# Optimization experiments

Hardware: AMD Instinct MI355X
Metric: run time of the kernel (lower is better)

Reference implementation:

```python
import jax, jax.numpy as jnp
import numpy as np

jax.config.update("jax_enable_x64", True)  # original computes distances in float64

B, NL, NP, C, H, G, A, E = 16, 64, 512, 128, 256, 10, 14, 2048
BN_EPS = 1e-5


def _static_indices():
    # ragged graph sizes (batch_num_nodes) -> static scatter / valid-pair indices
    counts_l = np.array([32 if i % 2 == 0 else 64 for i in range(B)])
    counts_p = np.array([256 if i % 2 == 0 else 512 for i in range(B)])
    idx_l = np.concatenate([b * NL + np.arange(c) for b, c in enumerate(counts_l)])
    idx_p = np.concatenate([b * NP + np.arange(c) for b, c in enumerate(counts_p)])
    mask_l = np.zeros(B * NL, bool); mask_l[idx_l] = True
    mask_p = np.zeros(B * NP, bool); mask_p[idx_p] = True
    mask = mask_l.reshape(B, NL, 1) & mask_p.reshape(B, 1, NP)  # C_mask
    pair_flat = np.nonzero(mask.reshape(-1))[0]                 # row-major == torch C[C_mask] order
    pb = pair_flat // (NL * NP)
    rem = pair_flat % (NL * NP)
    pair_l = pb * NL + rem // NP
    pair_p = pb * NP + rem % NP
    return idx_l, idx_p, pair_flat, pair_l, pair_p, pb, len(idx_l), len(idx_p)


def setup_inputs() -> dict:
    idx_l, idx_p, pair_flat, pair_l, pair_p, pair_b, TL, TP = _static_indices()
    ks = jax.random.split(jax.random.key(0), 14)
    f32 = jnp.float32
    s = 0.02
    return {
        "h_l": jax.random.normal(ks[0], (TL, C), f32),
        "h_p": jax.random.normal(ks[1], (TP, C), f32),
        "lig_pos": jax.random.normal(ks[2], (TL, 3), f32) * 5.0,
        "prot_pos": jax.random.normal(ks[3], (TP, A, 3), f32) * 5.0,
        "edge_src": jax.random.randint(ks[4], (E,), 0, TL),
        "edge_dst": jax.random.randint(ks[5], (E,), 0, TL),
        "idx_l": jnp.asarray(idx_l), "idx_p": jnp.asarray(idx_p),
        "pair_flat": jnp.asarray(pair_flat), "pair_l": jnp.asarray(pair_l),
        "pair_p": jnp.asarray(pair_p), "pair_b": jnp.asarray(pair_b),
        "W1": jax.random.normal(ks[6], (2 * C, H), f32) * s, "b1": jnp.zeros(H, f32),
        "gamma": jnp.ones(H, f32), "beta": jnp.zeros(H, f32),
        "rmean": jnp.zeros(H, f32), "rvar": jnp.ones(H, f32),
        "Wpi": jax.random.normal(ks[7], (H, G * A), f32) * s, "bpi": jnp.zeros(G * A, f32),
        "Wsig": jax.random.normal(ks[8], (H, G * A), f32) * s, "bsig": jnp.zeros(G * A, f32),
        "Wmu": jax.random.normal(ks[9], (H, G * A), f32) * s, "bmu": jnp.zeros(G * A, f32),
        "Wat": jax.random.normal(ks[10], (C, 17), f32) * s, "bat": jnp.zeros(17, f32),
        "Wbt": jax.random.normal(ks[11], (2 * C, 5), f32) * s, "bbt": jnp.zeros(5, f32),
    }


def reference(h_l, h_p, lig_pos, prot_pos, edge_src, edge_dst, idx_l, idx_p,
              pair_flat, pair_l, pair_p, pair_b, W1, b1, gamma, beta, rmean, rvar,
              Wpi, bpi, Wsig, bsig, Wmu, bmu, Wat, bat, Wbt, bbt):
    # scatter ragged node feats into padded dense batches (to_dense_batch_dgl)
    dense_l = jnp.zeros((B * NL, C), h_l.dtype).at[idx_l].set(h_l)
    dense_p = jnp.zeros((B * NP, C), h_p.dtype).at[idx_p].set(h_p)
    # gather only valid (ligand, protein) pairs instead of the dense [B,NL,NP,2C] tensor
    Cpair = jnp.concatenate([dense_l[pair_l], dense_p[pair_p]], axis=-1)  # [M, 2C]
    x = Cpair @ W1 + b1
    x = gamma * (x - rmean) / jnp.sqrt(rvar + BN_EPS) + beta  # BatchNorm1d (eval)
    x = jax.nn.elu(x)                                          # dropout off (eval)
    pi = jax.nn.softmax(x @ Wpi + bpi, axis=-1).reshape(-1, G, A)
    sigma = (jax.nn.elu(x @ Wsig + bsig) + 1.1).reshape(-1, G, A)
    mu = (jax.nn.elu(x @ Wmu + bmu) + 1.0).reshape(-1, G, A)
    atom_types = h_l @ Wat + bat                               # [TL, 17]
    bond_types = jnp.concatenate([h_l[edge_src], h_l[edge_dst]], -1) @ Wbt + bbt  # [E, 5]
    # euclidean distance matrix in float64, as in the original
    X = jnp.zeros((B * NL, 3), jnp.float64).at[idx_l].set(lig_pos.astype(jnp.float64)).reshape(B, NL, 3)
    Y = jnp.zeros((B * NP, A, 3), jnp.float64).at[idx_p].set(prot_pos.astype(jnp.float64)).reshape(B, NP * A, 3)
    d2 = (-2.0 * jnp.einsum('bld,bpd->blp', X, Y)
          + jnp.sum(Y * Y, -1)[:, None, :] + jnp.sum(X * X, -1)[:, :, None])
    dist = jnp.nan_to_num(jnp.sqrt(d2), nan=10000.0).reshape(B * NL * NP, A)[pair_flat]
    dist = jax.lax.stop_gradient(dist[:, None, :])             # [M, 1, A], detached
    return (pi, sigma, mu, dist, atom_types, bond_types, pair_b)
```

## Files before the change

### kernel.cpp

```cpp
#include <hip/hip_runtime.h>


typedef __attribute__((ext_vector_type(4))) float f32x4;
typedef __attribute__((ext_vector_type(4))) unsigned int u32x4;
typedef __attribute__((ext_vector_type(8))) short bf16x8;

#define M_TOT 327680
#define WSCALE 16.0f
#define WDESCALE 0.0625f

__device__ __forceinline__ unsigned short f2bf(float f) {
    union { float f; unsigned int u; } v; v.f = f;
    unsigned int r = (v.u + 0x7FFFu + ((v.u >> 16) & 1u)) >> 16;
    return (unsigned short)r;
}

__device__ __forceinline__ float eluf(float y) {
    return fmaxf(y, 0.f) + __expf(fminf(y, 0.f)) - 1.f;
}

__device__ __forceinline__ float bfhalf_lo(unsigned int u) {
    return __uint_as_float(u << 16);
}
__device__ __forceinline__ float bfhalf_hi(unsigned int u) {
    return __uint_as_float(u & 0xFFFF0000u);
}

__device__ __forceinline__ void pair_decode(int m0, int& b, int& cl, int& cp0) {
    unsigned int P = (unsigned int)m0 / 40960u;
    unsigned int r = (unsigned int)m0 % 40960u;
    if (r < 8192u) {
        b = 2 * (int)P; cl = 96 * (int)P + (int)(r >> 8); cp0 = 768 * (int)P + (int)(r & 255u);
    } else {
        unsigned int rr = r - 8192u;
        b = 2 * (int)P + 1; cl = 96 * (int)P + 32 + (int)(rr >> 9);
        cp0 = 768 * (int)P + 256 + (int)(rr & 511u);
    }
}

__global__ void setup_kernel(const float* __restrict__ W1, const float* __restrict__ b1,
                             const float* __restrict__ gamma, const float* __restrict__ beta,
                             const float* __restrict__ rmean, const float* __restrict__ rvar,
                             const float* __restrict__ Wpi, const float* __restrict__ bpi,
                             const float* __restrict__ Wsig, const float* __restrict__ bsig,
                             const float* __restrict__ Wmu, const float* __restrict__ bmu,
                             const float* __restrict__ h_l,
                             const int* __restrict__ esrc, const int* __restrict__ edst,
                             const float* __restrict__ Wat, const float* __restrict__ bat,
                             const float* __restrict__ Wbt, const float* __restrict__ bbt,
                             const float* __restrict__ lig_pos, const float* __restrict__ prot_pos,
                             unsigned short* __restrict__ W1T, unsigned char* __restrict__ W2q,
                             float* __restrict__ b2s, float* __restrict__ a1v, float* __restrict__ csv,
                             float* __restrict__ out_at, float* __restrict__ out_bt,
                             float* __restrict__ out_dist, float* __restrict__ out_pb) {
    if (blockIdx.x >= 432) {
        const int m0 = (blockIdx.x - 432) * 256;
        int b, cl, cp0;
        pair_decode(m0, b, cl, cp0);
        const int rw = threadIdx.x;
        float lx = lig_pos[cl * 3 + 0];
        float ly = lig_pos[cl * 3 + 1];
        float lz = lig_pos[cl * 3 + 2];
        const float* pp = prot_pos + (size_t)(cp0 + rw) * 42;
        float* dr = out_dist + (size_t)(m0 + rw) * 14;
        #pragma unroll
        for (int a = 0; a < 14; ++a) {
            float dx = lx - pp[a * 3 + 0];
            float dy = ly - pp[a * 3 + 1];
            float dz = lz - pp[a * 3 + 2];
            dr[a] = sqrtf(dx * dx + dy * dy + dz * dz);
        }
        out_pb[m0 + rw] = (float)b;
        return;
    }

    int idx = blockIdx.x * 256 + threadIdx.x;
    {
        int j    = idx & 7;
        int h    = (idx >> 3) & 1;
        int lane = (idx >> 4) & 63;
        int sp   = (idx >> 10) & 3;
        int t    = idx >> 12;
        int f    = t % 9;
        int head = t / 9;
        int k    = (sp * 2 + h) * 32 + (lane >> 4) * 8 + j;
        int col  = f * 16 + (lane & 15);
        float v = 0.f;
        if (col < 140) {
            const float* Wh = (head == 0) ? Wpi : (head == 1) ? Wsig : Wmu;
            v = Wh[k * 140 + col] * WSCALE;
        }
        W2q[idx] = (unsigned char)(__builtin_amdgcn_cvt_pk_fp8_f32(v, 0.f, 0, false) & 0xFF);
    }
    if (idx < 256 * 256) {
        int n = idx & 255, k = idx >> 8;
        W1T[n * 256 + k] = f2bf(W1[k * 256 + n]);
    }
    if (idx < 432) {
        int head = idx / 144, col = idx % 144;
        float v = 0.f;
        if (col < 140) v = (head == 0) ? bpi[col] : (head == 1) ? bsig[col] : bmu[col];
        b2s[idx] = v * WSCALE;
    }
    if (idx < 256) {
        float s = gamma[idx] * rsqrtf(rvar[idx] + 1e-5f);
        a1v[idx] = s;
        csv[idx] = s * (b1[idx] - rmean[idx]) + beta[idx];
    }
    if (idx < 768 * 17) {
        int row = idx / 17, c = idx % 17;
        const float* hr = h_l + (size_t)row * 128;
        float s = bat[c];
        #pragma unroll 4
        for (int k = 0; k < 128; ++k) s += hr[k] * Wat[k * 17 + c];
        out_at[idx] = s;
    } else if (idx < 768 * 17 + 2048 * 5) {
        int t2 = idx - 768 * 17;
        int e = t2 / 5, c = t2 % 5;
        const float* hs = h_l + (size_t)esrc[e] * 128;
        const float* hd = h_l + (size_t)edst[e] * 128;
        float s = bbt[c];
        #pragma unroll 4
        for (int k = 0; k < 128; ++k)
            s += hs[k] * Wbt[k * 5 + c] + hd[k] * Wbt[(k + 128) * 5 + c];
        out_bt[t2] = s;
    }
}

__global__ __launch_bounds__(256, 2) void node_gemm(
        const float* __restrict__ h_l, const float* __restrict__ h_p,
        const unsigned short* __restrict__ W1T,
        const float* __restrict__ a1v, const float* __restrict__ csv,
        unsigned short* __restrict__ Lq, unsigned short* __restrict__ Pq) {
    const int tid = threadIdx.x, lane = tid & 63, w = tid >> 6;
    const int cGrp = lane & 15, g = lane >> 4;
    const int nh   = blockIdx.x & 1;
    const int row0 = (blockIdx.x >> 1) * 64;
    const bool isLig = row0 < 768;
    const float* src = isLig ? (h_l + (size_t)row0 * 128) : (h_p + (size_t)(row0 - 768) * 128);
    unsigned short* dst = isLig ? (Lq + (size_t)row0 * 256) : (Pq + (size_t)(row0 - 768) * 256);
    const int koff = isLig ? 0 : 128;

    f32x4 acc[8];
    #pragma unroll
    for (int fn = 0; fn < 8; ++fn) acc[fn] = (f32x4){0.f, 0.f, 0.f, 0.f};

    #pragma unroll
    for (int fk = 0; fk < 4; ++fk) {
        const float* ap = src + (size_t)(w * 16 + cGrp) * 128 + fk * 32 + g * 8;
        f32x4 qa = *(const f32x4*)ap;
        f32x4 qb = *(const f32x4*)(ap + 4);
        bf16x8 af;
        af[0] = (short)f2bf(qa[0]); af[1] = (short)f2bf(qa[1]);
        af[2] = (short)f2bf(qa[2]); af[3] = (short)f2bf(qa[3]);
        af[4] = (short)f2bf(qb[0]); af[5] = (short)f2bf(qb[1]);
        af[6] = (short)f2bf(qb[2]); af[7] = (short)f2bf(qb[3]);
        #pragma unroll
        for (int fn = 0; fn < 8; ++fn) {
            int n = nh * 128 + fn * 16 + cGrp;
            bf16x8 bf = *(const bf16x8*)(W1T + (size_t)n * 256 + koff + fk * 32 + g * 8);
            acc[fn] = __builtin_amdgcn_mfma_f32_16x16x32_bf16(af, bf, acc[fn], 0, 0, 0);
        }
    }
    #pragma unroll
    for (int fn = 0; fn < 8; ++fn) {
        int h = nh * 128 + fn * 16 + cGrp;
        float s = a1v[h];
        float c0 = isLig ? csv[h] : 0.f;
        #pragma unroll
        for (int rg = 0; rg < 4; ++rg)
            dst[(size_t)(w * 16 + g * 4 + rg) * 256 + h] = f2bf(s * acc[fn][rg] + c0);
    }
}

__global__ __launch_bounds__(256, 4) void pair_kernel(
        const unsigned short* __restrict__ Lq, const unsigned short* __restrict__ Pq,
        const unsigned char* __restrict__ W2q, const float* __restrict__ b2s,
        float* __restrict__ out_pi, float* __restrict__ out_sig, float* __restrict__ out_mu) {

    __shared__ __align__(16) unsigned char Bs[36864];

    const int tid = threadIdx.x, lane = tid & 63, w = tid >> 6;
    const int c = lane & 15, g = lane >> 4;
    const int m0 = blockIdx.x * 64;

    int b, cl, cp0;
    pair_decode(m0, b, cl, cp0);

    u32x4 stg[9];
    #pragma unroll
    for (int i = 0; i < 9; ++i)
        stg[i] = *(const u32x4*)(W2q + (size_t)(tid + 256 * i) * 16);

    const int row = w * 16 + c;
    const unsigned short* pqp = Pq + (size_t)(cp0 + row) * 256;
    const unsigned short* lqp = Lq + (size_t)cl * 256;
    long Xa[8];
    #pragma unroll
    for (int s = 0; s < 8; ++s) {
        u32x4 pv = *(const u32x4*)(pqp + s * 32 + g * 8);
        u32x4 lv = *(const u32x4*)(lqp + s * 32 + g * 8);
        float y0 = eluf(bfhalf_lo(pv[0]) + bfhalf_lo(lv[0]));
        float y1 = eluf(bfhalf_hi(pv[0]) + bfhalf_hi(lv[0]));
        float y2 = eluf(bfhalf_lo(pv[1]) + bfhalf_lo(lv[1]));
        float y3 = eluf(bfhalf_hi(pv[1]) + bfhalf_hi(lv[1]));
        float y4 = eluf(bfhalf_lo(pv[2]) + bfhalf_lo(lv[2]));
        float y5 = eluf(bfhalf_hi(pv[2]) + bfhalf_hi(lv[2]));
        float y6 = eluf(bfhalf_lo(pv[3]) + bfhalf_lo(lv[3]));
        float y7 = eluf(bfhalf_hi(pv[3]) + bfhalf_hi(lv[3]));
        unsigned int lo = (unsigned int)__builtin_amdgcn_cvt_pk_fp8_f32(y0, y1, 0, false);
        lo = (unsigned int)__builtin_amdgcn_cvt_pk_fp8_f32(y2, y3, (int)lo, true);
        unsigned int hi = (unsigned int)__builtin_amdgcn_cvt_pk_fp8_f32(y4, y5, 0, false);
        hi = (unsigned int)__builtin_amdgcn_cvt_pk_fp8_f32(y6, y7, (int)hi, true);
        Xa[s] = (long)(((unsigned long long)hi << 32) | (unsigned long long)lo);
    }

    const bool v8 = (c < 12);

    #pragma unroll
    for (int head = 0; head < 3; ++head) {
        #pragma unroll
        for (int i = 0; i < 9; ++i)
            *(u32x4*)(Bs + (size_t)(tid + 256 * i) * 16) = stg[i];
        __syncthreads();

        float bb[9];
        #pragma unroll
        for (int f = 0; f < 9; ++f) bb[f] = b2s[head * 144 + f * 16 + c];

        f32x4 acc[9];
        #pragma unroll
        for (int f = 0; f < 9; ++f) acc[f] = (f32x4){bb[f], bb[f], bb[f], bb[f]};

        #pragma unroll
        for (int sp = 0; sp < 4; ++sp) {
            long xa0 = Xa[2 * sp], xa1 = Xa[2 * sp + 1];
            #pragma unroll
            for (int f = 0; f < 9; ++f) {
                u32x4 bq = *(const u32x4*)(Bs + f * 4096 + sp * 1024 + lane * 16);
                long b0 = (long)(((unsigned long long)bq[1] << 32) | (unsigned long long)bq[0]);
                long b1 = (long)(((unsigned long long)bq[3] << 32) | (unsigned long long)bq[2]);
                acc[f] = __builtin_amdgcn_mfma_f32_16x16x32_fp8_fp8(xa0, b0, acc[f], 0, 0, 0);
                acc[f] = __builtin_amdgcn_mfma_f32_16x16x32_fp8_fp8(xa1, b1, acc[f], 0, 0, 0);
            }
        }

        if (head < 2) {
            const unsigned char* wsrc = W2q + (size_t)(head + 1) * 36864;
            #pragma unroll
            for (int i = 0; i < 9; ++i)
                stg[i] = *(const u32x4*)(wsrc + (size_t)(tid + 256 * i) * 16);
        }

        #pragma unroll
        for (int f = 0; f < 9; ++f)
            #pragma unroll
            for (int q = 0; q < 4; ++q) acc[f][q] *= WDESCALE;

        if (head == 0) {
            #pragma unroll
            for (int q = 0; q < 4; ++q) {
                float e0 = __expf(acc[0][q]), e1 = __expf(acc[1][q]);
                float e2 = __expf(acc[2][q]), e3 = __expf(acc[3][q]);
                float e4 = __expf(acc[4][q]), e5 = __expf(acc[5][q]);
                float e6 = __expf(acc[6][q]), e7 = __expf(acc[7][q]);
                float e8 = v8 ? __expf(acc[8][q]) : 0.f;
                float sm = ((e0 + e1) + (e2 + e3)) + ((e4 + e5) + (e6 + e7)) + e8;
                sm += __shfl_xor(sm, 1, 64);
                sm += __shfl_xor(sm, 2, 64);
                sm += __shfl_xor(sm, 4, 64);
                sm += __shfl_xor(sm, 8, 64);
                float inv = 1.f / sm;
                acc[0][q] = e0 * inv; acc[1][q] = e1 * inv;
                acc[2][q] = e2 * inv; acc[3][q] = e3 * inv;
                acc[4][q] = e4 * inv; acc[5][q] = e5 * inv;
                acc[6][q] = e6 * inv; acc[7][q] = e7 * inv;
                acc[8][q] = e8 * inv;
            }
        } else {
            const float addc = (head == 1) ? 1.1f : 1.0f;
            #pragma unroll
            for (int f = 0; f < 9; ++f)
                #pragma unroll
                for (int q = 0; q < 4; ++q) acc[f][q] = eluf(acc[f][q]) + addc;
        }

        __syncthreads();
        float* ot = (float*)Bs;
        {
            const int rbase = (w * 16 + g * 4) * 140 + c;
            #pragma unroll
            for (int f = 0; f < 9; ++f) {
                if (f < 8 || v8) {
                    #pragma unroll
                    for (int q = 0; q < 4; ++q)
                        ot[rbase + q * 140 + f * 16] = acc[f][q];
                }
            }
        }
        __syncthreads();

        float* dsth = (head == 0) ? out_pi : (head == 1) ? out_sig : out_mu;
        float* dst = dsth + (size_t)m0 * 140;
        #pragma unroll
        for (int i = 0; i < 9; ++i) {
            int idx = tid + 256 * i;
            if (idx < 2240)
                *(f32x4*)(dst + idx * 4) = *(const f32x4*)(ot + idx * 4);
        }

        if (head < 2) __syncthreads();
    }
}

extern "C" void kernel_launch(void* const* d_in, const int* in_sizes, int n_in,
                              void* d_out, int out_size, void* d_ws, size_t ws_size,
                              hipStream_t stream) {
    const float* h_l      = (const float*)d_in[0];
    const float* h_p      = (const float*)d_in[1];
    const float* lig_pos  = (const float*)d_in[2];
    const float* prot_pos = (const float*)d_in[3];
    const int*   esrc     = (const int*)d_in[4];
    const int*   edst     = (const int*)d_in[5];
    const float* W1    = (const float*)d_in[12];
    const float* b1    = (const float*)d_in[13];
    const float* gamma = (const float*)d_in[14];
    const float* beta  = (const float*)d_in[15];
    const float* rmean = (const float*)d_in[16];
    const float* rvar  = (const float*)d_in[17];
    const float* Wpi   = (const float*)d_in[18];
    const float* bpi   = (const float*)d_in[19];
    const float* Wsig  = (const float*)d_in[20];
    const float* bsig  = (const float*)d_in[21];
    const float* Wmu   = (const float*)d_in[22];
    const float* bmu   = (const float*)d_in[23];
    const float* Wat   = (const float*)d_in[24];
    const float* bat   = (const float*)d_in[25];
    const float* Wbt   = (const float*)d_in[26];
    const float* bbt   = (const float*)d_in[27];

    char* ws = (char*)d_ws;
    unsigned short* W1T = (unsigned short*)(ws + 0);
    unsigned char*  W2q = (unsigned char*)(ws + 131072);
    float*          b2s = (float*)(ws + 241664);
    float*          a1v = (float*)(ws + 243392);
    float*          csv = (float*)(ws + 244416);
    unsigned short* Lq  = (unsigned short*)(ws + 245440);
    unsigned short* Pq  = (unsigned short*)(ws + 638656);

    float* out = (float*)d_out;
    const size_t M = M_TOT;
    float* out_pi   = out;
    float* out_sig  = out + M * 140;
    float* out_mu   = out + 2 * M * 140;
    float* out_dist = out + 3 * M * 140;
    float* out_at   = out + 3 * M * 140 + M * 14;
    float* out_bt   = out_at + 768 * 17;
    float* out_pb   = out_bt + 2048 * 5;

    hipLaunchKernelGGL(setup_kernel, dim3(432 + M_TOT / 256), dim3(256), 0, stream,
                       W1, b1, gamma, beta, rmean, rvar,
                       Wpi, bpi, Wsig, bsig, Wmu, bmu,
                       h_l, esrc, edst, Wat, bat, Wbt, bbt,
                       lig_pos, prot_pos,
                       W1T, W2q, b2s, a1v, csv, out_at, out_bt, out_dist, out_pb);

    hipLaunchKernelGGL(node_gemm, dim3(2 * (768 + 6144) / 64), dim3(256), 0, stream,
                       h_l, h_p, W1T, a1v, csv, Lq, Pq);

    hipLaunchKernelGGL(pair_kernel, dim3(M_TOT / 64), dim3(256), 0, stream,
                       Lq, Pq, W2q, b2s, out_pi, out_sig, out_mu);
}
```

Measured before the change: 176.4 us.

## Fold node GEMM into setup kernel with per-block LDS W1 transpose

Merges the node_gemm kernel into setup_kernel as extra blocks. Each node block converts and transposes its 128x128 slice of W1 to bf16 in shared memory and computes the batch-norm scale and shift inline, instead of reading a global W1T and the a1v/csv buffers produced by the setup pass. This removes one kernel launch and the dependency between the two kernels, letting the node GEMM overlap with the distance and prep work. The cost is redundant W1 conversion in every node block and 34KB of LDS allocated for all blocks of setup_kernel, which may lower occupancy for the distance blocks.

```diff
diff --git a/kernel.cpp b/kernel.cpp
--- a/kernel.cpp
+++ b/kernel.cpp
@@ -8,6 +8,10 @@
 #define M_TOT 327680
 #define WSCALE 16.0f
 #define WDESCALE 0.0625f
+
+#define NODE_BLOCKS 216
+#define PREP_BLOCKS 432
+#define DIST_BLOCKS 1280
 
 __device__ __forceinline__ unsigned short f2bf(float f) {
     union { float f; unsigned int u; } v; v.f = f;
@@ -44,20 +48,80 @@
                              const float* __restrict__ Wpi, const float* __restrict__ bpi,
                              const float* __restrict__ Wsig, const float* __restrict__ bsig,
                              const float* __restrict__ Wmu, const float* __restrict__ bmu,
-                             const float* __restrict__ h_l,
+                             const float* __restrict__ h_l, const float* __restrict__ h_p,
                              const int* __restrict__ esrc, const int* __restrict__ edst,
                              const float* __restrict__ Wat, const float* __restrict__ bat,
                              const float* __restrict__ Wbt, const float* __restrict__ bbt,
                              const float* __restrict__ lig_pos, const float* __restrict__ prot_pos,
-                             unsigned short* __restrict__ W1T, unsigned char* __restrict__ W2q,
-                             float* __restrict__ b2s, float* __restrict__ a1v, float* __restrict__ csv,
+                             unsigned char* __restrict__ W2q, float* __restrict__ b2s,
+                             unsigned short* __restrict__ Lq, unsigned short* __restrict__ Pq,
                              float* __restrict__ out_at, float* __restrict__ out_bt,
                              float* __restrict__ out_dist, float* __restrict__ out_pb) {
-    if (blockIdx.x >= 432) {
-        const int m0 = (blockIdx.x - 432) * 256;
+
+    __shared__ __align__(16) unsigned short Wl[128 * 136];
+
+    const int bid = blockIdx.x;
+    const int tid = threadIdx.x;
+
+    if (bid < NODE_BLOCKS) {
+        const int nh   = bid & 1;
+        const int row0 = (bid >> 1) * 64;
+        const bool isLig = row0 < 768;
+        const float* src = isLig ? (h_l + (size_t)row0 * 128) : (h_p + (size_t)(row0 - 768) * 128);
+        unsigned short* dst = isLig ? (Lq + (size_t)row0 * 256) : (Pq + (size_t)(row0 - 768) * 256);
+        const int koff = isLig ? 0 : 128;
+
+        {
+            const int nn = tid & 127;
+            const int kb = tid >> 7;
+            #pragma unroll 8
+            for (int i = 0; i < 64; ++i) {
+                int kk = i * 2 + kb;
+                Wl[nn * 136 + kk] = f2bf(W1[(size_t)(koff + kk) * 256 + nh * 128 + nn]);
+            }
+        }
+        __syncthreads();
+
+        const int lane = tid & 63, w = tid >> 6;
+        const int cGrp = lane & 15, g = lane >> 4;
+
+        f32x4 acc[8];
+        #pragma unroll
+        for (int fn = 0; fn < 8; ++fn) acc[fn] = (f32x4){0.f, 0.f, 0.f, 0.f};
+
+        #pragma unroll
+        for (int fk = 0; fk < 4; ++fk) {
+            const float* ap = src + (size_t)(w * 16 + cGrp) * 128 + fk * 32 + g * 8;
+            f32x4 qa = *(const f32x4*)ap;
+            f32x4 qb = *(const f32x4*)(ap + 4);
+            bf16x8 af;
+            af[0] = (short)f2bf(qa[0]); af[1] = (short)f2bf(qa[1]);
+            af[2] = (short)f2bf(qa[2]); af[3] = (short)f2bf(qa[3]);
+            af[4] = (short)f2bf(qb[0]); af[5] = (short)f2bf(qb[1]);
+            af[6] = (short)f2bf(qb[2]); af[7] = (short)f2bf(qb[3]);
+            #pragma unroll
+            for (int fn = 0; fn < 8; ++fn) {
+                bf16x8 bf = *(const bf16x8*)(Wl + (fn * 16 + cGrp) * 136 + fk * 32 + g * 8);
+                acc[fn] = __builtin_amdgcn_mfma_f32_16x16x32_bf16(af, bf, acc[fn], 0, 0, 0);
+            }
+        }
+        #pragma unroll
+        for (int fn = 0; fn < 8; ++fn) {
+            int h = nh * 128 + fn * 16 + cGrp;
+            float s  = gamma[h] * rsqrtf(rvar[h] + 1e-5f);
+            float c0 = isLig ? (s * (b1[h] - rmean[h]) + beta[h]) : 0.f;
+            #pragma unroll
+            for (int rg = 0; rg < 4; ++rg)
+                dst[(size_t)(w * 16 + g * 4 + rg) * 256 + h] = f2bf(s * acc[fn][rg] + c0);
+        }
+        return;
+    }
+
+    if (bid >= NODE_BLOCKS + PREP_BLOCKS) {
+        const int m0 = (bid - NODE_BLOCKS - PREP_BLOCKS) * 256;
         int b, cl, cp0;
         pair_decode(m0, b, cl, cp0);
-        const int rw = threadIdx.x;
+        const int rw = tid;
         float lx = lig_pos[cl * 3 + 0];
         float ly = lig_pos[cl * 3 + 1];
         float lz = lig_pos[cl * 3 + 2];
@@ -74,7 +138,7 @@
         return;
     }
 
-    int idx = blockIdx.x * 256 + threadIdx.x;
+    int idx = (bid - NODE_BLOCKS) * 256 + tid;
     {
         int j    = idx & 7;
         int h    = (idx >> 3) & 1;
@@ -92,20 +156,11 @@
         }
         W2q[idx] = (unsigned char)(__builtin_amdgcn_cvt_pk_fp8_f32(v, 0.f, 0, false) & 0xFF);
     }
-    if (idx < 256 * 256) {
-        int n = idx & 255, k = idx >> 8;
-        W1T[n * 256 + k] = f2bf(W1[k * 256 + n]);
-    }
     if (idx < 432) {
         int head = idx / 144, col = idx % 144;
         float v = 0.f;
         if (col < 140) v = (head == 0) ? bpi[col] : (head == 1) ? bsig[col] : bmu[col];
         b2s[idx] = v * WSCALE;
-    }
-    if (idx < 256) {
-        float s = gamma[idx] * rsqrtf(rvar[idx] + 1e-5f);
-        a1v[idx] = s;
-        csv[idx] = s * (b1[idx] - rmean[idx]) + beta[idx];
     }
     if (idx < 768 * 17) {
         int row = idx / 17, c = idx % 17;
@@ -124,52 +179,6 @@
         for (int k = 0; k < 128; ++k)
             s += hs[k] * Wbt[k * 5 + c] + hd[k] * Wbt[(k + 128) * 5 + c];
         out_bt[t2] = s;
-    }
-}
-
-__global__ __launch_bounds__(256, 2) void node_gemm(
-        const float* __restrict__ h_l, const float* __restrict__ h_p,
-        const unsigned short* __restrict__ W1T,
-        const float* __restrict__ a1v, const float* __restrict__ csv,
-        unsigned short* __restrict__ Lq, unsigned short* __restrict__ Pq) {
-    const int tid = threadIdx.x, lane = tid & 63, w = tid >> 6;
-    const int cGrp = lane & 15, g = lane >> 4;
-    const int nh   = blockIdx.x & 1;
-    const int row0 = (blockIdx.x >> 1) * 64;
-    const bool isLig = row0 < 768;
-    const float* src = isLig ? (h_l + (size_t)row0 * 128) : (h_p + (size_t)(row0 - 768) * 128);
-    unsigned short* dst = isLig ? (Lq + (size_t)row0 * 256) : (Pq + (size_t)(row0 - 768) * 256);
-    const int koff = isLig ? 0 : 128;
-
-    f32x4 acc[8];
-    #pragma unroll
-    for (int fn = 0; fn < 8; ++fn) acc[fn] = (f32x4){0.f, 0.f, 0.f, 0.f};
-
-    #pragma unroll
-    for (int fk = 0; fk < 4; ++fk) {
-        const float* ap = src + (size_t)(w * 16 + cGrp) * 128 + fk * 32 + g * 8;
-        f32x4 qa = *(const f32x4*)ap;
-        f32x4 qb = *(const f32x4*)(ap + 4);
-        bf16x8 af;
-        af[0] = (short)f2bf(qa[0]); af[1] = (short)f2bf(qa[1]);
-        af[2] = (short)f2bf(qa[2]); af[3] = (short)f2bf(qa[3]);
-        af[4] = (short)f2bf(qb[0]); af[5] = (short)f2bf(qb[1]);
-        af[6] = (short)f2bf(qb[2]); af[7] = (short)f2bf(qb[3]);
-        #pragma unroll
-        for (int fn = 0; fn < 8; ++fn) {
-            int n = nh * 128 + fn * 16 + cGrp;
-            bf16x8 bf = *(const bf16x8*)(W1T + (size_t)n * 256 + koff + fk * 32 + g * 8);
-            acc[fn] = __builtin_amdgcn_mfma_f32_16x16x32_bf16(af, bf, acc[fn], 0, 0, 0);
-        }
-    }
-    #pragma unroll
-    for (int fn = 0; fn < 8; ++fn) {
-        int h = nh * 128 + fn * 16 + cGrp;
-        float s = a1v[h];
-        float c0 = isLig ? csv[h] : 0.f;
-        #pragma unroll
-        for (int rg = 0; rg < 4; ++rg)
-            dst[(size_t)(w * 16 + g * 4 + rg) * 256 + h] = f2bf(s * acc[fn][rg] + c0);
     }
 }
 
@@ -340,11 +349,8 @@
     const float* bbt   = (const float*)d_in[27];
 
     char* ws = (char*)d_ws;
-    unsigned short* W1T = (unsigned short*)(ws + 0);
     unsigned char*  W2q = (unsigned char*)(ws + 131072);
     float*          b2s = (float*)(ws + 241664);
-    float*          a1v = (float*)(ws + 243392);
-    float*          csv = (float*)(ws + 244416);
     unsigned short* Lq  = (unsigned short*)(ws + 245440);
     unsigned short* Pq  = (unsigned short*)(ws + 638656);
 
@@ -358,15 +364,12 @@
     float* out_bt   = out_at + 768 * 17;
     float* out_pb   = out_bt + 2048 * 5;
 
-    hipLaunchKernelGGL(setup_kernel, dim3(432 + M_TOT / 256), dim3(256), 0, stream,
+    hipLaunchKernelGGL(setup_kernel, dim3(NODE_BLOCKS + PREP_BLOCKS + DIST_BLOCKS), dim3(256), 0, stream,
                        W1, b1, gamma, beta, rmean, rvar,
                        Wpi, bpi, Wsig, bsig, Wmu, bmu,
-                       h_l, esrc, edst, Wat, bat, Wbt, bbt,
+                       h_l, h_p, esrc, edst, Wat, bat, Wbt, bbt,
                        lig_pos, prot_pos,
-                       W1T, W2q, b2s, a1v, csv, out_at, out_bt, out_dist, out_pb);
-
-    hipLaunchKernelGGL(node_gemm, dim3(2 * (768 + 6144) / 64), dim3(256), 0, stream,
-                       h_l, h_p, W1T, a1v, csv, Lq, Pq);
+                       W2q, b2s, Lq, Pq, out_at, out_bt, out_dist, out_pb);
 
     hipLaunchKernelGGL(pair_kernel, dim3(M_TOT / 64), dim3(256), 0, stream,
                        Lq, Pq, W2q, b2s, out_pi, out_sig, out_mu);
```

Measured after the change: 166.8 us (median of 2 runs). 1.06x faster.
